# Optimization experiments

Hardware: AMD Instinct MI355X
Metric: run time of the kernel (lower is better)

The kernel has to match this reference:

```python
import jax, jax.numpy as jnp
import numpy as np

N = 20000            # nodes
E = 320000           # edges (before self loops)
NUM_PLAYERS = 5000
FEAT = 64            # feature_dim
H = 128              # hidden_dim
OUT = 10             # out_features
NEG_SLOPE = 0.2


def _p(key, shape, fan_in):
    return jax.random.normal(key, shape, dtype=jnp.float32) / np.sqrt(fan_in)


def setup_inputs() -> dict:
    key = jax.random.key(0)
    ks = jax.random.split(key, 20)
    # x_player: col 0 = player id (stored as float), cols 1: = features
    ids = jax.random.randint(ks[0], (N, 1), 0, NUM_PLAYERS + 1).astype(jnp.float32)
    feats = jax.random.normal(ks[1], (N, FEAT), dtype=jnp.float32)
    x_player = jnp.concatenate([ids, feats], axis=1)
    edge_index = jax.random.randint(ks[2], (2, E), 0, N, dtype=jnp.int32)
    return {
        "x_player": x_player,
        "edge_index": edge_index,
        "emb": jax.random.normal(ks[3], (NUM_PLAYERS + 1, H), dtype=jnp.float32),
        "proj_W": _p(ks[4], (H + FEAT, H), H + FEAT),
        "proj_b": jnp.zeros((H,), jnp.float32),
        "W1l": _p(ks[5], (H, 4 * H), H),
        "W1r": _p(ks[6], (H, 4 * H), H),
        "att1": _p(ks[7], (4, H), H),
        "b1": jnp.zeros((4 * H,), jnp.float32),
        "W2l": _p(ks[8], (4 * H, H), 4 * H),
        "W2r": _p(ks[9], (4 * H, H), 4 * H),
        "att2": _p(ks[10], (1, H), H),
        "b2": jnp.zeros((H,), jnp.float32),
        "out_W": _p(ks[11], (H, OUT), H),
        "out_b": jnp.zeros((OUT,), jnp.float32),
    }


def gatv2(x, src, dst, Wl, Wr, att, bias, heads, ch, concat):
    # GATv2Conv (PyG defaults: share_weights=False, negative_slope=0.2,
    # add_self_loops handled by caller, dropout off at eval)
    xl = (x @ Wl).reshape(N, heads, ch)   # source transform (x_j)
    xr = (x @ Wr).reshape(N, heads, ch)   # target transform (x_i)
    h = xl[src] + xr[dst]                                      # [E,H,C]
    e = jnp.sum(jax.nn.leaky_relu(h, NEG_SLOPE) * att, -1)     # [E,H]
    # segment softmax over incoming edges of each dst node
    m = jax.ops.segment_max(e, dst, num_segments=N)            # [N,H]
    ex = jnp.exp(e - m[dst])
    s = jax.ops.segment_sum(ex, dst, num_segments=N)
    alpha = ex / (s[dst] + 1e-16)                              # [E,H]
    out = jax.ops.segment_sum(alpha[..., None] * xl[src], dst, num_segments=N)
    out = out.reshape(N, heads * ch) if concat else out.mean(axis=1)
    return out + bias


def reference(x_player, edge_index, emb, proj_W, proj_b,
              W1l, W1r, att1, b1, W2l, W2r, att2, b2, out_W, out_b):
    ids = x_player[:, 0].astype(jnp.int32)
    combined = jnp.concatenate([emb[ids], x_player[:, 1:]], axis=1)
    x = jax.nn.relu(combined @ proj_W + proj_b)                # [N,H]
    # add self loops (GATv2Conv default)
    loop = jnp.arange(N, dtype=edge_index.dtype)
    src = jnp.concatenate([edge_index[0], loop])
    dst = jnp.concatenate([edge_index[1], loop])
    x = jax.nn.relu(gatv2(x, src, dst, W1l, W1r, att1, b1, 4, H, True))
    x = gatv2(x, src, dst, W2l, W2r, att2, b2, 1, H, True)
    return x @ out_W + out_b                                   # [N,OUT]
```

## Files before the change

### kernel.cpp

```cpp
#include <hip/hip_runtime.h>
#include <math.h>

#define NNODES 20000
#define XP_COLS 65

typedef unsigned int uint32;
typedef __attribute__((ext_vector_type(8))) short short8;
typedef __attribute__((ext_vector_type(4))) float float4v;

__device__ __forceinline__ float bflo(uint32 u){ return __uint_as_float(u << 16); }
__device__ __forceinline__ float bfhi(uint32 u){ return __uint_as_float(u & 0xffff0000u); }
__device__ __forceinline__ unsigned short f2bf(float f){
  uint32 u = __float_as_uint(f);
  uint32 r = (u + 0x7fffu + ((u >> 16) & 1u)) >> 16;
  return (unsigned short)r;
}
__device__ __forceinline__ void unpack8(uint4 u, float* x){
  x[0]=bflo(u.x); x[1]=bfhi(u.x); x[2]=bflo(u.y); x[3]=bfhi(u.y);
  x[4]=bflo(u.z); x[5]=bfhi(u.z); x[6]=bflo(u.w); x[7]=bfhi(u.w);
}
__device__ __forceinline__ float rowsum16(float x){
  x += __int_as_float(__builtin_amdgcn_update_dpp(0, __float_as_int(x), 0x121, 0xf, 0xf, true));
  x += __int_as_float(__builtin_amdgcn_update_dpp(0, __float_as_int(x), 0x122, 0xf, 0xf, true));
  x += __int_as_float(__builtin_amdgcn_update_dpp(0, __float_as_int(x), 0x124, 0xf, 0xf, true));
  x += __int_as_float(__builtin_amdgcn_update_dpp(0, __float_as_int(x), 0x128, 0xf, 0xf, true));
  return x;
}

__global__ void k_cvt_count(const int* __restrict__ dst, int E, int* __restrict__ deg,
                            const float* __restrict__ W1l, const float* __restrict__ W1r,
                            const float* __restrict__ W2l, const float* __restrict__ W2r,
                            const float* __restrict__ projW,
                            unsigned short* __restrict__ T1l, unsigned short* __restrict__ T1r,
                            unsigned short* __restrict__ T2l, unsigned short* __restrict__ T2r,
                            unsigned short* __restrict__ Tp){
  int gid = blockIdx.x * 256 + threadIdx.x;
  if (gid < E){
    atomicAdd(&deg[dst[gid]], 1);
    return;
  }
  int idx = gid - E;
  if (idx < 65536){
    int o = idx;
    int n = o >> 7, k = o & 127;
    T1l[o] = f2bf(W1l[k * 512 + n]);
  } else if (idx < 131072){
    int o = idx - 65536;
    int n = o >> 7, k = o & 127;
    T1r[o] = f2bf(W1r[k * 512 + n]);
  } else if (idx < 196608){
    int o = idx - 131072;
    int n = o >> 9, k = o & 511;
    T2l[o] = f2bf(W2l[k * 128 + n]);
  } else if (idx < 262144){
    int o = idx - 196608;
    int n = o >> 9, k = o & 511;
    T2r[o] = f2bf(W2r[k * 128 + n]);
  } else if (idx < 286720){
    int o = idx - 262144;
    int n = o / 192, k = o - n * 192;
    Tp[o] = f2bf(projW[k * 128 + n]);
  }
}

__global__ __launch_bounds__(256) void k_scan(const int* __restrict__ deg,
                                              int* __restrict__ off,
                                              int* __restrict__ cursor){
  const int CH = 80;
  int tid = threadIdx.x;
  int lane = tid & 63, w = tid >> 6;
  int beg = tid * CH;
  bool act = beg < NNODES;
  int sum = 0;
  if (act){
    const int4* p = (const int4*)(deg + beg);
    #pragma unroll
    for (int i = 0; i < 20; i++){
      int4 v = p[i];
      sum += v.x + v.y + v.z + v.w + 4;
    }
  }
  int inc = sum;
  #pragma unroll
  for (int d = 1; d < 64; d <<= 1){
    int t = __shfl_up(inc, d, 64);
    if (lane >= d) inc += t;
  }
  __shared__ int wtot[4];
  if (lane == 63) wtot[w] = inc;
  __syncthreads();
  int wbase = 0;
  for (int i = 0; i < w; i++) wbase += wtot[i];
  int run = wbase + inc - sum;
  if (act){
    const int4* p = (const int4*)(deg + beg);
    int4* po = (int4*)(off + beg);
    int4* pc = (int4*)(cursor + beg);
    #pragma unroll
    for (int i = 0; i < 20; i++){
      int4 v = p[i];
      int4 o;
      o.x = run; run += v.x + 1;
      o.y = run; run += v.y + 1;
      o.z = run; run += v.z + 1;
      o.w = run; run += v.w + 1;
      po[i] = o; pc[i] = o;
    }
  }
  if (tid == 249) off[NNODES] = run;
}

__global__ void k_fill(const int* __restrict__ src, const int* __restrict__ dst, int E,
                       int* __restrict__ cursor, int* __restrict__ csr){
  int t = blockIdx.x * 256 + threadIdx.x;
  if (t < NNODES){
    int p = atomicAdd(&cursor[t], 1);
    csr[p] = t;
  } else if (t < NNODES + E){
    int e = t - NNODES;
    int p = atomicAdd(&cursor[dst[e]], 1);
    csr[p] = src[e];
  }
}

__global__ __launch_bounds__(256) void k_proj_mfma(const float* __restrict__ xp,
                                                   const float* __restrict__ emb,
                                                   const unsigned short* __restrict__ Bt,
                                                   const float* __restrict__ bias,
                                                   unsigned short* __restrict__ Xb){
  __shared__ unsigned short As[64][40];
  __shared__ unsigned short Bs[128][40];
  __shared__ int ids[64];
  int tid = threadIdx.x;
  int bm = blockIdx.x * 64;
  int w = tid >> 6, lane = tid & 63;
  int wm = (w >> 1) * 32, wn = (w & 1) * 64;
  int quad = lane >> 4, l16 = lane & 15;
  if (tid < 64){
    int g = bm + tid;
    ids[tid] = (g < NNODES) ? (int)xp[(size_t)g * XP_COLS] : 0;
  }
  float4v acc[2][4];
  #pragma unroll
  for (int i = 0; i < 2; i++)
    #pragma unroll
    for (int j = 0; j < 4; j++) acc[i][j] = (float4v){0.f,0.f,0.f,0.f};
  int am = tid >> 2, ak = (tid & 3) * 8;
  int gm = bm + am;
  bool mv = gm < NNODES;
  int brow = tid >> 1, bk = (tid & 1) * 16;
  __syncthreads();

  for (int k0 = 0; k0 < 192; k0 += 32){
    float v[8];
    if (k0 < 128){
      const float* ep = emb + (size_t)ids[am] * 128 + k0 + ak;
      float4 e0 = *(const float4*)ep;
      float4 e1 = *(const float4*)(ep + 4);
      v[0]=e0.x; v[1]=e0.y; v[2]=e0.z; v[3]=e0.w;
      v[4]=e1.x; v[5]=e1.y; v[6]=e1.z; v[7]=e1.w;
    } else {
      const float* fp = xp + (size_t)gm * XP_COLS + 1 + (k0 - 128) + ak;
      #pragma unroll
      for (int i = 0; i < 8; i++) v[i] = mv ? fp[i] : 0.f;
    }
    ushort4 o0, o1;
    o0.x=f2bf(v[0]); o0.y=f2bf(v[1]); o0.z=f2bf(v[2]); o0.w=f2bf(v[3]);
    o1.x=f2bf(v[4]); o1.y=f2bf(v[5]); o1.z=f2bf(v[6]); o1.w=f2bf(v[7]);
    *(ushort4*)&As[am][ak]     = o0;
    *(ushort4*)&As[am][ak + 4] = o1;
    const unsigned short* bp = Bt + (size_t)brow * 192 + k0 + bk;
    *(uint4*)&Bs[brow][bk]     = *(const uint4*)bp;
    *(uint4*)&Bs[brow][bk + 8] = *(const uint4*)(bp + 8);
    __syncthreads();
    short8 af[2], bf[4];
    #pragma unroll
    for (int t = 0; t < 2; t++) af[t] = *(const short8*)&As[wm + t * 16 + l16][quad * 8];
    #pragma unroll
    for (int t = 0; t < 4; t++) bf[t] = *(const short8*)&Bs[wn + t * 16 + l16][quad * 8];
    #pragma unroll
    for (int tm = 0; tm < 2; tm++)
      #pragma unroll
      for (int tn = 0; tn < 4; tn++)
        acc[tm][tn] = __builtin_amdgcn_mfma_f32_16x16x32_bf16(af[tm], bf[tn], acc[tm][tn], 0, 0, 0);
    __syncthreads();
  }
  #pragma unroll
  for (int tm = 0; tm < 2; tm++){
    #pragma unroll
    for (int r = 0; r < 4; r++){
      int row = bm + wm + tm * 16 + quad * 4 + r;
      if (row >= NNODES) continue;
      #pragma unroll
      for (int tn = 0; tn < 4; tn++){
        int col = wn + tn * 16 + l16;
        float val = fmaxf(acc[tm][tn][r] + bias[col], 0.f);
        Xb[(size_t)row * 128 + col] = f2bf(val);
      }
    }
  }
}

template<int K, int N, int MODE, int NH>
__global__ __launch_bounds__(256) void k_mfma(const unsigned short* __restrict__ A,
                                              const unsigned short* __restrict__ B0t,
                                              const unsigned short* __restrict__ B1t,
                                              void* __restrict__ C0, void* __restrict__ C1,
                                              const float* __restrict__ att,
                                              float* __restrict__ dl, float* __restrict__ dr,
                                              int* __restrict__ gmax){
  const unsigned short* Bt = blockIdx.z ? B1t : B0t;
  __shared__ unsigned short As[64][40];
  __shared__ unsigned short Bs[128][40];
  __shared__ float red[4][32];
  __shared__ float redu[4][32];
  int tid = threadIdx.x;
  int bm = blockIdx.y * 64;
  int bn = blockIdx.x * 128;
  int head = (NH == 1) ? 0 : blockIdx.x;
  int w = tid >> 6, lane = tid & 63;
  int wm = (w >> 1) * 32, wn = (w & 1) * 64;
  int quad = lane >> 4, l16 = lane & 15;
  float av[4], aav[4];
  #pragma unroll
  for (int tn = 0; tn < 4; tn++){
    av[tn] = att[head * 128 + wn + tn * 16 + l16];
    aav[tn] = fabsf(av[tn]);
  }
  float4v acc[2][4];
  #pragma unroll
  for (int i = 0; i < 2; i++)
    #pragma unroll
    for (int j = 0; j < 4; j++) acc[i][j] = (float4v){0.f,0.f,0.f,0.f};
  int am = tid >> 2, ak = (tid & 3) * 8;
  int gm = bm + am;
  bool mv = gm < NNODES;
  int brow = tid >> 1, bk = (tid & 1) * 16;

  for (int k0 = 0; k0 < K; k0 += 32){
    uint4 va = {0u,0u,0u,0u};
    if (mv) va = *(const uint4*)(A + (size_t)gm * K + k0 + ak);
    *(uint4*)&As[am][ak] = va;
    const unsigned short* bp = Bt + (size_t)(bn + brow) * K + k0 + bk;
    *(uint4*)&Bs[brow][bk]     = *(const uint4*)bp;
    *(uint4*)&Bs[brow][bk + 8] = *(const uint4*)(bp + 8);
    __syncthreads();
    short8 af[2], bf[4];
    #pragma unroll
    for (int t = 0; t < 2; t++) af[t] = *(const short8*)&As[wm + t * 16 + l16][quad * 8];
    #pragma unroll
    for (int t = 0; t < 4; t++) bf[t] = *(const short8*)&Bs[wn + t * 16 + l16][quad * 8];
    #pragma unroll
    for (int tm = 0; tm < 2; tm++)
      #pragma unroll
      for (int tn = 0; tn < 4; tn++)
        acc[tm][tn] = __builtin_amdgcn_mfma_f32_16x16x32_bf16(af[tm], bf[tn], acc[tm][tn], 0, 0, 0);
    __syncthreads();
  }
  #pragma unroll
  for (int tm = 0; tm < 2; tm++){
    #pragma unroll
    for (int r = 0; r < 4; r++){
      int row = bm + wm + tm * 16 + quad * 4 + r;
      if (row < NNODES){
        #pragma unroll
        for (int tn = 0; tn < 4; tn++){
          int col = bn + wn + tn * 16 + l16;
          float val = acc[tm][tn][r];
          if (MODE == 0 || blockIdx.z == 0){
            unsigned short* C = (unsigned short*)(blockIdx.z ? C1 : C0);
            C[(size_t)row * N + col] = f2bf(val);
          } else {
            ((float*)C1)[(size_t)row * N + col] = val;
          }
        }
      }
      float pd = acc[tm][0][r] * av[0];
      pd = fmaf(acc[tm][1][r], av[1], pd);
      pd = fmaf(acc[tm][2][r], av[2], pd);
      pd = fmaf(acc[tm][3][r], av[3], pd);
      float pu = fabsf(acc[tm][0][r]) * aav[0];
      pu = fmaf(fabsf(acc[tm][1][r]), aav[1], pu);
      pu = fmaf(fabsf(acc[tm][2][r]), aav[2], pu);
      pu = fmaf(fabsf(acc[tm][3][r]), aav[3], pu);
      pd = rowsum16(pd);
      pu = rowsum16(pu);
      if (l16 == 0){
        red[w][tm * 16 + quad * 4 + r]  = pd;
        redu[w][tm * 16 + quad * 4 + r] = pu;
      }
    }
  }
  __syncthreads();
  if (tid < 64){
    float vd, vu;
    if (tid < 32){ vd = red[0][tid] + red[1][tid];   vu = redu[0][tid] + redu[1][tid]; }
    else { vd = red[2][tid & 31] + red[3][tid & 31]; vu = redu[2][tid & 31] + redu[3][tid & 31]; }
    int row = bm + tid;
    bool ok = row < NNODES;
    if (ok){
      float* D = blockIdx.z ? dr : dl;
      D[row * NH + head] = vd;
    }
    if (blockIdx.z == 0){
      float v = ok ? fmaf(0.4f, vu, 0.6f * vd) : -4.0e6f;
      #pragma unroll
      for (int dd = 1; dd < 64; dd <<= 1) v = fmaxf(v, __shfl_xor(v, dd));
      if (tid == 0) atomicMax(&gmax[head], (int)ceilf(v * 256.0f) + (1 << 30));
    }
  }
}

__device__ __forceinline__ void attn1_batch(const uint4* u, const float* d,
                                            const float* r, const float* a, float base,
                                            float& s, float* acc){
  float x0[8], x1[8], x2[8], x3[8];
  unpack8(u[0], x0); unpack8(u[1], x1); unpack8(u[2], x2); unpack8(u[3], x3);
  float p0 = 0.f, p1 = 0.f, p2 = 0.f, p3 = 0.f;
  #pragma unroll
  for (int i = 0; i < 8; i++){
    p0 = fmaf(a[i], fabsf(x0[i] + r[i]), p0);
    p1 = fmaf(a[i], fabsf(x1[i] + r[i]), p1);
    p2 = fmaf(a[i], fabsf(x2[i] + r[i]), p2);
    p3 = fmaf(a[i], fabsf(x3[i] + r[i]), p3);
  }
  p0 = rowsum16(p0); p1 = rowsum16(p1); p2 = rowsum16(p2); p3 = rowsum16(p3);
  float ex0 = __expf(fmaf(0.4f, p0, fmaf(0.6f, d[0], base)));
  float ex1 = __expf(fmaf(0.4f, p1, fmaf(0.6f, d[1], base)));
  float ex2 = __expf(fmaf(0.4f, p2, fmaf(0.6f, d[2], base)));
  float ex3 = __expf(fmaf(0.4f, p3, fmaf(0.6f, d[3], base)));
  s += (ex0 + ex1) + (ex2 + ex3);
  #pragma unroll
  for (int i = 0; i < 8; i++){
    float t = fmaf(ex0, x0[i], ex1 * x1[i]);
    t = fmaf(ex2, x2[i], t);
    acc[i] = fmaf(ex3, x3[i], acc[i] + t);
  }
}

__global__ __launch_bounds__(1024) void k_attn1(const unsigned short* __restrict__ xl,
                                                const unsigned short* __restrict__ xr,
                                                const float* __restrict__ dl, const float* __restrict__ dr,
                                                const float* __restrict__ att, const float* __restrict__ bias,
                                                const int* __restrict__ gmax,
                                                const int* __restrict__ off, const int* __restrict__ csr,
                                                unsigned short* __restrict__ out){
  int lane = threadIdx.x & 63;
  int n = blockIdx.x * 16 + (threadIdx.x >> 6);
  int h = lane >> 4;
  uint4 ur = *(const uint4*)(xr + (size_t)n * 512 + lane * 8);
  float r[8]; unpack8(ur, r);
  const float* ap = att + lane * 8;
  float4 A0 = *(const float4*)ap, A1 = *(const float4*)(ap + 4);
  float a[8] = {A0.x,A0.y,A0.z,A0.w,A1.x,A1.y,A1.z,A1.w};
  float V = 0.f;
  #pragma unroll
  for (int i = 0; i < 8; i++) V = fmaf(fabsf(a[i]), fabsf(r[i]), V);
  V = rowsum16(V);
  float Mg = (float)(gmax[h] - (1 << 30)) * (1.0f / 256.0f);
  float base = fmaf(0.6f, dr[n * 4 + h], -Mg - 0.4f * V);
  int beg = off[n], end = off[n + 1];
  int cnt = end - beg;
  int nfull = cnt >> 2;

  float s = 0.f;
  float acc[8] = {0,0,0,0,0,0,0,0};
  uint4 uA[4], uB[4];
  float dA[4], dB[4];
  int j = beg;
  if (nfull > 0){
    int s0 = csr[j], s1 = csr[j+1], s2 = csr[j+2], s3 = csr[j+3];
    uA[0] = *(const uint4*)(xl + (size_t)s0 * 512 + lane * 8);
    uA[1] = *(const uint4*)(xl + (size_t)s1 * 512 + lane * 8);
    uA[2] = *(const uint4*)(xl + (size_t)s2 * 512 + lane * 8);
    uA[3] = *(const uint4*)(xl + (size_t)s3 * 512 + lane * 8);
    dA[0] = dl[s0*4+h]; dA[1] = dl[s1*4+h]; dA[2] = dl[s2*4+h]; dA[3] = dl[s3*4+h];
  }
  for (int b = 0; b < nfull; b++){
    int jn = j + 4;
    if (b + 1 < nfull){
      int s0 = csr[jn], s1 = csr[jn+1], s2 = csr[jn+2], s3 = csr[jn+3];
      uB[0] = *(const uint4*)(xl + (size_t)s0 * 512 + lane * 8);
      uB[1] = *(const uint4*)(xl + (size_t)s1 * 512 + lane * 8);
      uB[2] = *(const uint4*)(xl + (size_t)s2 * 512 + lane * 8);
      uB[3] = *(const uint4*)(xl + (size_t)s3 * 512 + lane * 8);
      dB[0] = dl[s0*4+h]; dB[1] = dl[s1*4+h]; dB[2] = dl[s2*4+h]; dB[3] = dl[s3*4+h];
    }
    attn1_batch(uA, dA, r, a, base, s, acc);
    j = jn;
    #pragma unroll
    for (int i = 0; i < 4; i++){ uA[i] = uB[i]; dA[i] = dB[i]; }
  }
  for (; j < end; j++){
    int sn = csr[j];
    float dls = dl[sn * 4 + h];
    uint4 ux = *(const uint4*)(xl + (size_t)sn * 512 + lane * 8);
    float x[8]; unpack8(ux, x);
    float pa = 0.f, pb = 0.f;
    #pragma unroll
    for (int i = 0; i < 4; i++){
      pa = fmaf(a[i],     fabsf(x[i]     + r[i]),     pa);
      pb = fmaf(a[i + 4], fabsf(x[i + 4] + r[i + 4]), pb);
    }
    float p = rowsum16(pa + pb);
    float ex = __expf(fmaf(0.4f, p, fmaf(0.6f, dls, base)));
    s += ex;
    #pragma unroll
    for (int i = 0; i < 8; i++) acc[i] = fmaf(ex, x[i], acc[i]);
  }
  float inv = 1.f / (s + 1e-16f);
  const float* bp = bias + lane * 8;
  float4 B0 = *(const float4*)bp, B1 = *(const float4*)(bp + 4);
  float bb[8] = {B0.x,B0.y,B0.z,B0.w,B1.x,B1.y,B1.z,B1.w};
  unsigned short o[8];
  #pragma unroll
  for (int i = 0; i < 8; i++)
    o[i] = f2bf(fmaxf(fmaf(acc[i], inv, bb[i]), 0.f));
  uint4 ov;
  ov.x = (uint32)o[0] | ((uint32)o[1] << 16);
  ov.y = (uint32)o[2] | ((uint32)o[3] << 16);
  ov.z = (uint32)o[4] | ((uint32)o[5] << 16);
  ov.w = (uint32)o[6] | ((uint32)o[7] << 16);
  *(uint4*)(out + (size_t)n * 512 + lane * 8) = ov;
}

__device__ __forceinline__ float red64(float p){
  p = rowsum16(p);
  p += __shfl_xor(p, 16);
  p += __shfl_xor(p, 32);
  return p;
}
__device__ __forceinline__ void attn2_batch(const uint32* u, const float* d,
                                            float2 rv, float2 av, float base,
                                            float& s, float& a0, float& a1){
  float x00 = bflo(u[0]), x01 = bfhi(u[0]);
  float x10 = bflo(u[1]), x11 = bfhi(u[1]);
  float x20 = bflo(u[2]), x21 = bfhi(u[2]);
  float x30 = bflo(u[3]), x31 = bfhi(u[3]);
  float p0 = fmaf(av.x, fabsf(x00 + rv.x), av.y * fabsf(x01 + rv.y));
  float p1 = fmaf(av.x, fabsf(x10 + rv.x), av.y * fabsf(x11 + rv.y));
  float p2 = fmaf(av.x, fabsf(x20 + rv.x), av.y * fabsf(x21 + rv.y));
  float p3 = fmaf(av.x, fabsf(x30 + rv.x), av.y * fabsf(x31 + rv.y));
  p0 = red64(p0); p1 = red64(p1); p2 = red64(p2); p3 = red64(p3);
  float ex0 = __expf(fmaf(0.4f, p0, fmaf(0.6f, d[0], base)));
  float ex1 = __expf(fmaf(0.4f, p1, fmaf(0.6f, d[1], base)));
  float ex2 = __expf(fmaf(0.4f, p2, fmaf(0.6f, d[2], base)));
  float ex3 = __expf(fmaf(0.4f, p3, fmaf(0.6f, d[3], base)));
  s += (ex0 + ex1) + (ex2 + ex3);
  float t0 = fmaf(ex0, x00, ex1 * x10); t0 = fmaf(ex2, x20, t0);
  float t1 = fmaf(ex0, x01, ex1 * x11); t1 = fmaf(ex2, x21, t1);
  a0 = fmaf(ex3, x30, a0 + t0);
  a1 = fmaf(ex3, x31, a1 + t1);
}

__global__ __launch_bounds__(1024) void k_attn2(const unsigned short* __restrict__ xl,
                                                const float* __restrict__ xr,
                                                const float* __restrict__ dl, const float* __restrict__ dr,
                                                const float* __restrict__ att, const float* __restrict__ bias,
                                                const float* __restrict__ outW, const float* __restrict__ outb,
                                                const int* __restrict__ gmax,
                                                const int* __restrict__ off, const int* __restrict__ csr,
                                                float* __restrict__ out){
  __shared__ float Wsh[1280];
  int tid = threadIdx.x;
  for (int i = tid; i < 1280; i += 1024) Wsh[i] = outW[i];
  __syncthreads();
  int lane = tid & 63;
  int n = blockIdx.x * 16 + (tid >> 6);
  float2 rv = *(const float2*)(xr + (size_t)n * 128 + lane * 2);
  float2 av = *(const float2*)(att + lane * 2);
  float V = red64(fmaf(fabsf(av.x), fabsf(rv.x), fabsf(av.y) * fabsf(rv.y)));
  float Mg = (float)(gmax[0] - (1 << 30)) * (1.0f / 256.0f);
  float base = fmaf(0.6f, dr[n], -Mg - 0.4f * V);
  int beg = off[n], end = off[n + 1];
  int cnt = end - beg;
  int nfull = cnt >> 2;
  float s = 0.f;
  float a0 = 0.f, a1 = 0.f;
  uint32 uA[4], uB[4];
  float dA[4], dB[4];
  int j = beg;
  if (nfull > 0){
    int s0 = csr[j], s1 = csr[j+1], s2 = csr[j+2], s3 = csr[j+3];
    uA[0] = *(const uint32*)(xl + (size_t)s0 * 128 + lane * 2);
    uA[1] = *(const uint32*)(xl + (size_t)s1 * 128 + lane * 2);
    uA[2] = *(const uint32*)(xl + (size_t)s2 * 128 + lane * 2);
    uA[3] = *(const uint32*)(xl + (size_t)s3 * 128 + lane * 2);
    dA[0] = dl[s0]; dA[1] = dl[s1]; dA[2] = dl[s2]; dA[3] = dl[s3];
  }
  for (int b = 0; b < nfull; b++){
    int jn = j + 4;
    if (b + 1 < nfull){
      int s0 = csr[jn], s1 = csr[jn+1], s2 = csr[jn+2], s3 = csr[jn+3];
      uB[0] = *(const uint32*)(xl + (size_t)s0 * 128 + lane * 2);
      uB[1] = *(const uint32*)(xl + (size_t)s1 * 128 + lane * 2);
      uB[2] = *(const uint32*)(xl + (size_t)s2 * 128 + lane * 2);
      uB[3] = *(const uint32*)(xl + (size_t)s3 * 128 + lane * 2);
      dB[0] = dl[s0]; dB[1] = dl[s1]; dB[2] = dl[s2]; dB[3] = dl[s3];
    }
    attn2_batch(uA, dA, rv, av, base, s, a0, a1);
    j = jn;
    #pragma unroll
    for (int i = 0; i < 4; i++){ uA[i] = uB[i]; dA[i] = dB[i]; }
  }
  for (; j < end; j++){
    int sn = csr[j];
    float dls = dl[sn];
    uint32 u = *(const uint32*)(xl + (size_t)sn * 128 + lane * 2);
    float x0 = bflo(u), x1 = bfhi(u);
    float p = red64(fmaf(av.x, fabsf(x0 + rv.x), av.y * fabsf(x1 + rv.y)));
    float ex = __expf(fmaf(0.4f, p, fmaf(0.6f, dls, base)));
    s += ex;
    a0 = fmaf(ex, x0, a0);
    a1 = fmaf(ex, x1, a1);
  }
  float inv = 1.f / (s + 1e-16f);
  int c = lane * 2;
  float x2_0 = fmaf(a0, inv, bias[c]);
  float x2_1 = fmaf(a1, inv, bias[c + 1]);
  #pragma unroll
  for (int o = 0; o < 10; o++){
    float p = fmaf(x2_0, Wsh[c * 10 + o], x2_1 * Wsh[(c + 1) * 10 + o]);
    p = red64(p);
    if (lane == 0) out[(size_t)n * 10 + o] = p + outb[o];
  }
}

extern "C" void kernel_launch(void* const* d_in, const int* in_sizes, int n_in,
                              void* d_out, int out_size, void* d_ws, size_t ws_size,
                              hipStream_t stream){
  const float* xp    = (const float*)d_in[0];
  const int*   ei    = (const int*)  d_in[1];
  const float* emb   = (const float*)d_in[2];
  const float* projW = (const float*)d_in[3];
  const float* projb = (const float*)d_in[4];
  const float* W1l   = (const float*)d_in[5];
  const float* W1r   = (const float*)d_in[6];
  const float* att1  = (const float*)d_in[7];
  const float* b1    = (const float*)d_in[8];
  const float* W2l   = (const float*)d_in[9];
  const float* W2r   = (const float*)d_in[10];
  const float* att2  = (const float*)d_in[11];
  const float* b2    = (const float*)d_in[12];
  const float* outW  = (const float*)d_in[13];
  const float* outb  = (const float*)d_in[14];
  float* out = (float*)d_out;

  int E = in_sizes[1] / 2;
  const int* esrc = ei;
  const int* edst = ei + E;

  char* w = (char*)d_ws;
  int* gmaxi = (int*)w; w += 32;
  int* deg  = (int*)w; w += (size_t)NNODES * 4;
  int* off  = (int*)w; w += (size_t)(NNODES + 4) * 4;
  int* cur  = (int*)w; w += (size_t)NNODES * 4;
  int* csr  = (int*)w; w += (size_t)(NNODES + E) * 4;
  unsigned short* Xb   = (unsigned short*)w; w += (size_t)NNODES * 128 * 2;
  unsigned short* Wt1l = (unsigned short*)w; w += (size_t)512 * 128 * 2;
  unsigned short* Wt1r = (unsigned short*)w; w += (size_t)512 * 128 * 2;
  unsigned short* Wt2l = (unsigned short*)w; w += (size_t)128 * 512 * 2;
  unsigned short* Wt2r = (unsigned short*)w; w += (size_t)128 * 512 * 2;
  unsigned short* Wtp  = (unsigned short*)w; w += (size_t)128 * 192 * 2;
  unsigned short* xl1b = (unsigned short*)w; w += (size_t)NNODES * 512 * 2;
  unsigned short* xr1b = (unsigned short*)w; w += (size_t)NNODES * 512 * 2;
  unsigned short* X1b  = (unsigned short*)w; w += (size_t)NNODES * 512 * 2;
  unsigned short* xl2b = (unsigned short*)w; w += (size_t)NNODES * 128 * 2;
  float* xr2 = (float*)w; w += (size_t)NNODES * 128 * 4;
  float* dl1 = (float*)w; w += (size_t)NNODES * 4 * 4;
  float* dr1 = (float*)w; w += (size_t)NNODES * 4 * 4;
  float* dl2 = (float*)w; w += (size_t)NNODES * 4;
  float* dr2 = (float*)w; w += (size_t)NNODES * 4;

  hipMemsetAsync(gmaxi, 0, 32 + (size_t)NNODES * 4, stream);
  int cvt_total = E + 286720;
  k_cvt_count<<<(cvt_total + 255) / 256, 256, 0, stream>>>(
      edst, E, deg, W1l, W1r, W2l, W2r, projW, Wt1l, Wt1r, Wt2l, Wt2r, Wtp);
  k_scan<<<1, 256, 0, stream>>>(deg, off, cur);
  k_fill<<<(NNODES + E + 255) / 256, 256, 0, stream>>>(esrc, edst, E, cur, csr);

  k_proj_mfma<<<dim3((NNODES + 63) / 64), 256, 0, stream>>>(xp, emb, Wtp, projb, Xb);
  k_mfma<128, 512, 0, 4><<<dim3(4, (NNODES + 63) / 64, 2), 256, 0, stream>>>(
      Xb, Wt1l, Wt1r, xl1b, xr1b, att1, dl1, dr1, gmaxi);
  k_attn1<<<NNODES / 16, 1024, 0, stream>>>(xl1b, xr1b, dl1, dr1, att1, b1, gmaxi, off, csr, X1b);
  k_mfma<512, 128, 1, 1><<<dim3(1, (NNODES + 63) / 64, 2), 256, 0, stream>>>(
      X1b, Wt2l, Wt2r, xl2b, xr2, att2, dl2, dr2, gmaxi + 4);
  k_attn2<<<NNODES / 16, 1024, 0, stream>>>(xl2b, xr2, dl2, dr2, att2, b2, outW, outb, gmaxi + 4, off, csr, out);
}
```

Measured before the change: 287.5 us.

## Split each node's edge list across four waves in both attention kernels

Both attention kernels change from one wavefront per destination node (16 nodes per 1024-thread block) to one 256-thread block per node. The four waves each process a quarter of the incoming edges in masked groups of four, then combine partial sums and accumulators through shared memory. This gives more independent gathers in flight per node and shortens each wave's serial chain, aiming at latency-bound gather loops. In exchange it drops the software double-buffered prefetch, adds LDS reductions and a barrier per node, wastes lanes on masked padding for low-degree nodes, and launches 20000 small blocks.

```diff
diff --git a/kernel.cpp b/kernel.cpp
--- a/kernel.cpp
+++ b/kernel.cpp
@@ -25,6 +25,12 @@
   x += __int_as_float(__builtin_amdgcn_update_dpp(0, __float_as_int(x), 0x124, 0xf, 0xf, true));
   x += __int_as_float(__builtin_amdgcn_update_dpp(0, __float_as_int(x), 0x128, 0xf, 0xf, true));
   return x;
+}
+__device__ __forceinline__ float red64(float p){
+  p = rowsum16(p);
+  p += __shfl_xor(p, 16);
+  p += __shfl_xor(p, 32);
+  return p;
 }
 
 __global__ void k_cvt_count(const int* __restrict__ dst, int E, int* __restrict__ deg,
@@ -311,42 +317,16 @@
   }
 }
 
-__device__ __forceinline__ void attn1_batch(const uint4* u, const float* d,
-                                            const float* r, const float* a, float base,
-                                            float& s, float* acc){
-  float x0[8], x1[8], x2[8], x3[8];
-  unpack8(u[0], x0); unpack8(u[1], x1); unpack8(u[2], x2); unpack8(u[3], x3);
-  float p0 = 0.f, p1 = 0.f, p2 = 0.f, p3 = 0.f;
-  #pragma unroll
-  for (int i = 0; i < 8; i++){
-    p0 = fmaf(a[i], fabsf(x0[i] + r[i]), p0);
-    p1 = fmaf(a[i], fabsf(x1[i] + r[i]), p1);
-    p2 = fmaf(a[i], fabsf(x2[i] + r[i]), p2);
-    p3 = fmaf(a[i], fabsf(x3[i] + r[i]), p3);
-  }
-  p0 = rowsum16(p0); p1 = rowsum16(p1); p2 = rowsum16(p2); p3 = rowsum16(p3);
-  float ex0 = __expf(fmaf(0.4f, p0, fmaf(0.6f, d[0], base)));
-  float ex1 = __expf(fmaf(0.4f, p1, fmaf(0.6f, d[1], base)));
-  float ex2 = __expf(fmaf(0.4f, p2, fmaf(0.6f, d[2], base)));
-  float ex3 = __expf(fmaf(0.4f, p3, fmaf(0.6f, d[3], base)));
-  s += (ex0 + ex1) + (ex2 + ex3);
-  #pragma unroll
-  for (int i = 0; i < 8; i++){
-    float t = fmaf(ex0, x0[i], ex1 * x1[i]);
-    t = fmaf(ex2, x2[i], t);
-    acc[i] = fmaf(ex3, x3[i], acc[i] + t);
-  }
-}
-
-__global__ __launch_bounds__(1024) void k_attn1(const unsigned short* __restrict__ xl,
-                                                const unsigned short* __restrict__ xr,
-                                                const float* __restrict__ dl, const float* __restrict__ dr,
-                                                const float* __restrict__ att, const float* __restrict__ bias,
-                                                const int* __restrict__ gmax,
-                                                const int* __restrict__ off, const int* __restrict__ csr,
-                                                unsigned short* __restrict__ out){
-  int lane = threadIdx.x & 63;
-  int n = blockIdx.x * 16 + (threadIdx.x >> 6);
+__global__ __launch_bounds__(256) void k_attn1(const unsigned short* __restrict__ xl,
+                                               const unsigned short* __restrict__ xr,
+                                               const float* __restrict__ dl, const float* __restrict__ dr,
+                                               const float* __restrict__ att, const float* __restrict__ bias,
+                                               const int* __restrict__ gmax,
+                                               const int* __restrict__ off, const int* __restrict__ csr,
+                                               unsigned short* __restrict__ out){
+  int tid = threadIdx.x;
+  int w = tid >> 6, lane = tid & 63;
+  int n = blockIdx.x;
   int h = lane >> 4;
   uint4 ur = *(const uint4*)(xr + (size_t)n * 512 + lane * 8);
   float r[8]; unpack8(ur, r);
@@ -361,112 +341,79 @@
   float base = fmaf(0.6f, dr[n * 4 + h], -Mg - 0.4f * V);
   int beg = off[n], end = off[n + 1];
   int cnt = end - beg;
-  int nfull = cnt >> 2;
+  int per = (cnt + 3) >> 2;
+  int myBeg = beg + w * per;
+  int myEnd = myBeg + per; if (myEnd > end) myEnd = end;
 
   float s = 0.f;
   float acc[8] = {0,0,0,0,0,0,0,0};
-  uint4 uA[4], uB[4];
-  float dA[4], dB[4];
-  int j = beg;
-  if (nfull > 0){
-    int s0 = csr[j], s1 = csr[j+1], s2 = csr[j+2], s3 = csr[j+3];
-    uA[0] = *(const uint4*)(xl + (size_t)s0 * 512 + lane * 8);
-    uA[1] = *(const uint4*)(xl + (size_t)s1 * 512 + lane * 8);
-    uA[2] = *(const uint4*)(xl + (size_t)s2 * 512 + lane * 8);
-    uA[3] = *(const uint4*)(xl + (size_t)s3 * 512 + lane * 8);
-    dA[0] = dl[s0*4+h]; dA[1] = dl[s1*4+h]; dA[2] = dl[s2*4+h]; dA[3] = dl[s3*4+h];
-  }
-  for (int b = 0; b < nfull; b++){
-    int jn = j + 4;
-    if (b + 1 < nfull){
-      int s0 = csr[jn], s1 = csr[jn+1], s2 = csr[jn+2], s3 = csr[jn+3];
-      uB[0] = *(const uint4*)(xl + (size_t)s0 * 512 + lane * 8);
-      uB[1] = *(const uint4*)(xl + (size_t)s1 * 512 + lane * 8);
-      uB[2] = *(const uint4*)(xl + (size_t)s2 * 512 + lane * 8);
-      uB[3] = *(const uint4*)(xl + (size_t)s3 * 512 + lane * 8);
-      dB[0] = dl[s0*4+h]; dB[1] = dl[s1*4+h]; dB[2] = dl[s2*4+h]; dB[3] = dl[s3*4+h];
-    }
-    attn1_batch(uA, dA, r, a, base, s, acc);
-    j = jn;
-    #pragma unroll
-    for (int i = 0; i < 4; i++){ uA[i] = uB[i]; dA[i] = dB[i]; }
-  }
-  for (; j < end; j++){
-    int sn = csr[j];
-    float dls = dl[sn * 4 + h];
-    uint4 ux = *(const uint4*)(xl + (size_t)sn * 512 + lane * 8);
-    float x[8]; unpack8(ux, x);
-    float pa = 0.f, pb = 0.f;
-    #pragma unroll
-    for (int i = 0; i < 4; i++){
-      pa = fmaf(a[i],     fabsf(x[i]     + r[i]),     pa);
-      pb = fmaf(a[i + 4], fabsf(x[i + 4] + r[i + 4]), pb);
-    }
-    float p = rowsum16(pa + pb);
-    float ex = __expf(fmaf(0.4f, p, fmaf(0.6f, dls, base)));
-    s += ex;
-    #pragma unroll
-    for (int i = 0; i < 8; i++) acc[i] = fmaf(ex, x[i], acc[i]);
-  }
-  float inv = 1.f / (s + 1e-16f);
-  const float* bp = bias + lane * 8;
-  float4 B0 = *(const float4*)bp, B1 = *(const float4*)(bp + 4);
-  float bb[8] = {B0.x,B0.y,B0.z,B0.w,B1.x,B1.y,B1.z,B1.w};
-  unsigned short o[8];
-  #pragma unroll
-  for (int i = 0; i < 8; i++)
-    o[i] = f2bf(fmaxf(fmaf(acc[i], inv, bb[i]), 0.f));
-  uint4 ov;
-  ov.x = (uint32)o[0] | ((uint32)o[1] << 16);
-  ov.y = (uint32)o[2] | ((uint32)o[3] << 16);
-  ov.z = (uint32)o[4] | ((uint32)o[5] << 16);
-  ov.w = (uint32)o[6] | ((uint32)o[7] << 16);
-  *(uint4*)(out + (size_t)n * 512 + lane * 8) = ov;
-}
-
-__device__ __forceinline__ float red64(float p){
-  p = rowsum16(p);
-  p += __shfl_xor(p, 16);
-  p += __shfl_xor(p, 32);
-  return p;
-}
-__device__ __forceinline__ void attn2_batch(const uint32* u, const float* d,
-                                            float2 rv, float2 av, float base,
-                                            float& s, float& a0, float& a1){
-  float x00 = bflo(u[0]), x01 = bfhi(u[0]);
-  float x10 = bflo(u[1]), x11 = bfhi(u[1]);
-  float x20 = bflo(u[2]), x21 = bfhi(u[2]);
-  float x30 = bflo(u[3]), x31 = bfhi(u[3]);
-  float p0 = fmaf(av.x, fabsf(x00 + rv.x), av.y * fabsf(x01 + rv.y));
-  float p1 = fmaf(av.x, fabsf(x10 + rv.x), av.y * fabsf(x11 + rv.y));
-  float p2 = fmaf(av.x, fabsf(x20 + rv.x), av.y * fabsf(x21 + rv.y));
-  float p3 = fmaf(av.x, fabsf(x30 + rv.x), av.y * fabsf(x31 + rv.y));
-  p0 = red64(p0); p1 = red64(p1); p2 = red64(p2); p3 = red64(p3);
-  float ex0 = __expf(fmaf(0.4f, p0, fmaf(0.6f, d[0], base)));
-  float ex1 = __expf(fmaf(0.4f, p1, fmaf(0.6f, d[1], base)));
-  float ex2 = __expf(fmaf(0.4f, p2, fmaf(0.6f, d[2], base)));
-  float ex3 = __expf(fmaf(0.4f, p3, fmaf(0.6f, d[3], base)));
-  s += (ex0 + ex1) + (ex2 + ex3);
-  float t0 = fmaf(ex0, x00, ex1 * x10); t0 = fmaf(ex2, x20, t0);
-  float t1 = fmaf(ex0, x01, ex1 * x11); t1 = fmaf(ex2, x21, t1);
-  a0 = fmaf(ex3, x30, a0 + t0);
-  a1 = fmaf(ex3, x31, a1 + t1);
-}
-
-__global__ __launch_bounds__(1024) void k_attn2(const unsigned short* __restrict__ xl,
-                                                const float* __restrict__ xr,
-                                                const float* __restrict__ dl, const float* __restrict__ dr,
-                                                const float* __restrict__ att, const float* __restrict__ bias,
-                                                const float* __restrict__ outW, const float* __restrict__ outb,
-                                                const int* __restrict__ gmax,
-                                                const int* __restrict__ off, const int* __restrict__ csr,
-                                                float* __restrict__ out){
+  for (int j0 = myBeg; j0 < myEnd; j0 += 4){
+    int i1 = j0 + 1, i2 = j0 + 2, i3 = j0 + 3;
+    float m1 = 1.f, m2 = 1.f, m3 = 1.f;
+    if (i1 >= myEnd){ i1 = j0; m1 = 0.f; }
+    if (i2 >= myEnd){ i2 = j0; m2 = 0.f; }
+    if (i3 >= myEnd){ i3 = j0; m3 = 0.f; }
+    int s0 = csr[j0], s1 = csr[i1], s2 = csr[i2], s3 = csr[i3];
+    uint4 u0 = *(const uint4*)(xl + (size_t)s0 * 512 + lane * 8);
+    uint4 u1 = *(const uint4*)(xl + (size_t)s1 * 512 + lane * 8);
+    uint4 u2 = *(const uint4*)(xl + (size_t)s2 * 512 + lane * 8);
+    uint4 u3 = *(const uint4*)(xl + (size_t)s3 * 512 + lane * 8);
+    float d0 = dl[s0 * 4 + h], d1 = dl[s1 * 4 + h];
+    float d2 = dl[s2 * 4 + h], d3 = dl[s3 * 4 + h];
+    float x0[8], x1[8], x2[8], x3[8];
+    unpack8(u0, x0); unpack8(u1, x1); unpack8(u2, x2); unpack8(u3, x3);
+    float p0 = 0.f, p1 = 0.f, p2 = 0.f, p3 = 0.f;
+    #pragma unroll
+    for (int i = 0; i < 8; i++){
+      p0 = fmaf(a[i], fabsf(x0[i] + r[i]), p0);
+      p1 = fmaf(a[i], fabsf(x1[i] + r[i]), p1);
+      p2 = fmaf(a[i], fabsf(x2[i] + r[i]), p2);
+      p3 = fmaf(a[i], fabsf(x3[i] + r[i]), p3);
+    }
+    p0 = rowsum16(p0); p1 = rowsum16(p1); p2 = rowsum16(p2); p3 = rowsum16(p3);
+    float ex0 = __expf(fmaf(0.4f, p0, fmaf(0.6f, d0, base)));
+    float ex1 = __expf(fmaf(0.4f, p1, fmaf(0.6f, d1, base))) * m1;
+    float ex2 = __expf(fmaf(0.4f, p2, fmaf(0.6f, d2, base))) * m2;
+    float ex3 = __expf(fmaf(0.4f, p3, fmaf(0.6f, d3, base))) * m3;
+    s += (ex0 + ex1) + (ex2 + ex3);
+    #pragma unroll
+    for (int i = 0; i < 8; i++){
+      float t = fmaf(ex0, x0[i], ex1 * x1[i]);
+      t = fmaf(ex2, x2[i], t);
+      acc[i] = fmaf(ex3, x3[i], acc[i] + t);
+    }
+  }
+  __shared__ float accsh[4][512];
+  __shared__ float ssh[4][4];
+  *(float4*)&accsh[w][lane * 8]     = make_float4(acc[0], acc[1], acc[2], acc[3]);
+  *(float4*)&accsh[w][lane * 8 + 4] = make_float4(acc[4], acc[5], acc[6], acc[7]);
+  if ((lane & 15) == 0) ssh[w][h] = s;
+  __syncthreads();
+  for (int c = tid; c < 512; c += 256){
+    float v = (accsh[0][c] + accsh[1][c]) + (accsh[2][c] + accsh[3][c]);
+    int hh = c >> 7;
+    float sv = (ssh[0][hh] + ssh[1][hh]) + (ssh[2][hh] + ssh[3][hh]);
+    float o = v / (sv + 1e-16f) + bias[c];
+    out[(size_t)n * 512 + c] = f2bf(fmaxf(o, 0.f));
+  }
+}
+
+__global__ __launch_bounds__(256) void k_attn2(const unsigned short* __restrict__ xl,
+                                               const float* __restrict__ xr,
+                                               const float* __restrict__ dl, const float* __restrict__ dr,
+                                               const float* __restrict__ att, const float* __restrict__ bias,
+                                               const float* __restrict__ outW, const float* __restrict__ outb,
+                                               const int* __restrict__ gmax,
+                                               const int* __restrict__ off, const int* __restrict__ csr,
+                                               float* __restrict__ out){
   __shared__ float Wsh[1280];
+  __shared__ float accsh[4][128];
+  __shared__ float ssh[4];
+  __shared__ float x2sh[128];
   int tid = threadIdx.x;
-  for (int i = tid; i < 1280; i += 1024) Wsh[i] = outW[i];
-  __syncthreads();
-  int lane = tid & 63;
-  int n = blockIdx.x * 16 + (tid >> 6);
+  for (int i = tid; i < 1280; i += 256) Wsh[i] = outW[i];
+  int w = tid >> 6, lane = tid & 63;
+  int n = blockIdx.x;
   float2 rv = *(const float2*)(xr + (size_t)n * 128 + lane * 2);
   float2 av = *(const float2*)(att + lane * 2);
   float V = red64(fmaf(fabsf(av.x), fabsf(rv.x), fabsf(av.y) * fabsf(rv.y)));
@@ -474,55 +421,60 @@
   float base = fmaf(0.6f, dr[n], -Mg - 0.4f * V);
   int beg = off[n], end = off[n + 1];
   int cnt = end - beg;
-  int nfull = cnt >> 2;
-  float s = 0.f;
-  float a0 = 0.f, a1 = 0.f;
-  uint32 uA[4], uB[4];
-  float dA[4], dB[4];
-  int j = beg;
-  if (nfull > 0){
-    int s0 = csr[j], s1 = csr[j+1], s2 = csr[j+2], s3 = csr[j+3];
-    uA[0] = *(const uint32*)(xl + (size_t)s0 * 128 + lane * 2);
-    uA[1] = *(const uint32*)(xl + (size_t)s1 * 128 + lane * 2);
-    uA[2] = *(const uint32*)(xl + (size_t)s2 * 128 + lane * 2);
-    uA[3] = *(const uint32*)(xl + (size_t)s3 * 128 + lane * 2);
-    dA[0] = dl[s0]; dA[1] = dl[s1]; dA[2] = dl[s2]; dA[3] = dl[s3];
-  }
-  for (int b = 0; b < nfull; b++){
-    int jn = j + 4;
-    if (b + 1 < nfull){
-      int s0 = csr[jn], s1 = csr[jn+1], s2 = csr[jn+2], s3 = csr[jn+3];
-      uB[0] = *(const uint32*)(xl + (size_t)s0 * 128 + lane * 2);
-      uB[1] = *(const uint32*)(xl + (size_t)s1 * 128 + lane * 2);
-      uB[2] = *(const uint32*)(xl + (size_t)s2 * 128 + lane * 2);
-      uB[3] = *(const uint32*)(xl + (size_t)s3 * 128 + lane * 2);
-      dB[0] = dl[s0]; dB[1] = dl[s1]; dB[2] = dl[s2]; dB[3] = dl[s3];
-    }
-    attn2_batch(uA, dA, rv, av, base, s, a0, a1);
-    j = jn;
-    #pragma unroll
-    for (int i = 0; i < 4; i++){ uA[i] = uB[i]; dA[i] = dB[i]; }
-  }
-  for (; j < end; j++){
-    int sn = csr[j];
-    float dls = dl[sn];
-    uint32 u = *(const uint32*)(xl + (size_t)sn * 128 + lane * 2);
-    float x0 = bflo(u), x1 = bfhi(u);
-    float p = red64(fmaf(av.x, fabsf(x0 + rv.x), av.y * fabsf(x1 + rv.y)));
-    float ex = __expf(fmaf(0.4f, p, fmaf(0.6f, dls, base)));
-    s += ex;
-    a0 = fmaf(ex, x0, a0);
-    a1 = fmaf(ex, x1, a1);
-  }
-  float inv = 1.f / (s + 1e-16f);
-  int c = lane * 2;
-  float x2_0 = fmaf(a0, inv, bias[c]);
-  float x2_1 = fmaf(a1, inv, bias[c + 1]);
-  #pragma unroll
-  for (int o = 0; o < 10; o++){
-    float p = fmaf(x2_0, Wsh[c * 10 + o], x2_1 * Wsh[(c + 1) * 10 + o]);
-    p = red64(p);
-    if (lane == 0) out[(size_t)n * 10 + o] = p + outb[o];
+  int per = (cnt + 3) >> 2;
+  int myBeg = beg + w * per;
+  int myEnd = myBeg + per; if (myEnd > end) myEnd = end;
+  float s = 0.f, a0 = 0.f, a1 = 0.f;
+  for (int j0 = myBeg; j0 < myEnd; j0 += 4){
+    int i1 = j0 + 1, i2 = j0 + 2, i3 = j0 + 3;
+    float m1 = 1.f, m2 = 1.f, m3 = 1.f;
+    if (i1 >= myEnd){ i1 = j0; m1 = 0.f; }
+    if (i2 >= myEnd){ i2 = j0; m2 = 0.f; }
+    if (i3 >= myEnd){ i3 = j0; m3 = 0.f; }
+    int s0 = csr[j0], s1 = csr[i1], s2 = csr[i2], s3 = csr[i3];
+    uint32 u0 = *(const uint32*)(xl + (size_t)s0 * 128 + lane * 2);
+    uint32 u1 = *(const uint32*)(xl + (size_t)s1 * 128 + lane * 2);
+    uint32 u2 = *(const uint32*)(xl + (size_t)s2 * 128 + lane * 2);
+    uint32 u3 = *(const uint32*)(xl + (size_t)s3 * 128 + lane * 2);
+    float d0 = dl[s0], d1 = dl[s1], d2 = dl[s2], d3 = dl[s3];
+    float x00 = bflo(u0), x01 = bfhi(u0);
+    float x10 = bflo(u1), x11 = bfhi(u1);
+    float x20 = bflo(u2), x21 = bfhi(u2);
+    float x30 = bflo(u3), x31 = bfhi(u3);
+    float p0 = fmaf(av.x, fabsf(x00 + rv.x), av.y * fabsf(x01 + rv.y));
+    float p1 = fmaf(av.x, fabsf(x10 + rv.x), av.y * fabsf(x11 + rv.y));
+    float p2 = fmaf(av.x, fabsf(x20 + rv.x), av.y * fabsf(x21 + rv.y));
+    float p3 = fmaf(av.x, fabsf(x30 + rv.x), av.y * fabsf(x31 + rv.y));
+    p0 = red64(p0); p1 = red64(p1); p2 = red64(p2); p3 = red64(p3);
+    float ex0 = __expf(fmaf(0.4f, p0, fmaf(0.6f, d0, base)));
+    float ex1 = __expf(fmaf(0.4f, p1, fmaf(0.6f, d1, base))) * m1;
+    float ex2 = __expf(fmaf(0.4f, p2, fmaf(0.6f, d2, base))) * m2;
+    float ex3 = __expf(fmaf(0.4f, p3, fmaf(0.6f, d3, base))) * m3;
+    s += (ex0 + ex1) + (ex2 + ex3);
+    float t0 = fmaf(ex0, x00, ex1 * x10); t0 = fmaf(ex2, x20, t0);
+    float t1 = fmaf(ex0, x01, ex1 * x11); t1 = fmaf(ex2, x21, t1);
+    a0 = fmaf(ex3, x30, a0 + t0);
+    a1 = fmaf(ex3, x31, a1 + t1);
+  }
+  accsh[w][lane * 2]     = a0;
+  accsh[w][lane * 2 + 1] = a1;
+  if (lane == 0) ssh[w] = s;
+  __syncthreads();
+  if (tid < 128){
+    float v = (accsh[0][tid] + accsh[1][tid]) + (accsh[2][tid] + accsh[3][tid]);
+    float sv = (ssh[0] + ssh[1]) + (ssh[2] + ssh[3]);
+    x2sh[tid] = v / (sv + 1e-16f) + bias[tid];
+  }
+  __syncthreads();
+  if (w == 0){
+    int c = lane * 2;
+    float x0 = x2sh[c], x1 = x2sh[c + 1];
+    #pragma unroll
+    for (int o = 0; o < 10; o++){
+      float p = fmaf(x0, Wsh[c * 10 + o], x1 * Wsh[(c + 1) * 10 + o]);
+      p = red64(p);
+      if (lane == 0) out[(size_t)n * 10 + o] = p + outb[o];
+    }
   }
 }
 
@@ -582,8 +534,8 @@
   k_proj_mfma<<<dim3((NNODES + 63) / 64), 256, 0, stream>>>(xp, emb, Wtp, projb, Xb);
   k_mfma<128, 512, 0, 4><<<dim3(4, (NNODES + 63) / 64, 2), 256, 0, stream>>>(
       Xb, Wt1l, Wt1r, xl1b, xr1b, att1, dl1, dr1, gmaxi);
-  k_attn1<<<NNODES / 16, 1024, 0, stream>>>(xl1b, xr1b, dl1, dr1, att1, b1, gmaxi, off, csr, X1b);
+  k_attn1<<<NNODES, 256, 0, stream>>>(xl1b, xr1b, dl1, dr1, att1, b1, gmaxi, off, csr, X1b);
   k_mfma<512, 128, 1, 1><<<dim3(1, (NNODES + 63) / 64, 2), 256, 0, stream>>>(
       X1b, Wt2l, Wt2r, xl2b, xr2, att2, dl2, dr2, gmaxi + 4);
-  k_attn2<<<NNODES / 16, 1024, 0, stream>>>(xl2b, xr2, dl2, dr2, att2, b2, outW, outb, gmaxi + 4, off, csr, out);
-}
+  k_attn2<<<NNODES, 256, 0, stream>>>(xl2b, xr2, dl2, dr2, att2, b2, outW, outb, gmaxi + 4, off, csr, out);
+}
```

Measured after the change: 307.2 us. 6.8% more time.
